# Performance work log

Measured on AMD Instinct MI355X. Metric: run time of the kernel, lower is better.

The kernel has to match this reference:

```python
import jax, jax.numpy as jnp
import numpy as np

N_ITERS = 50

def sinkhorn_knopp(W, n_iters=N_ITERS):
    # Project W onto the Birkhoff polytope via alternating row/col normalization.
    W = jnp.abs(W) + 1e-8
    def body(i, W):
        W = W / jnp.sum(W, axis=-1, keepdims=True)  # row-normalize
        W = W / jnp.sum(W, axis=-2, keepdims=True)  # col-normalize
        return W
    return jax.lax.fori_loop(0, n_iters, body, W)

def setup_inputs() -> dict:
    key = jax.random.key(0)
    k1, k2, k3 = jax.random.split(key, 3)
    residual = jax.random.normal(k1, (2, 4096, 4096), dtype=jnp.float32)
    sublayer_out = jax.random.normal(k2, (2, 4096, 4096), dtype=jnp.float32)
    # Mimic init: eye(2)*2 + 0.01*randn
    W_raw = jnp.eye(2, dtype=jnp.float32) * 2.0 + 0.01 * jax.random.normal(k3, (2, 2), dtype=jnp.float32)
    return {"residual": residual, "sublayer_out": sublayer_out, "W_raw": W_raw}

def reference(residual, sublayer_out, W_raw):
    W = sinkhorn_knopp(W_raw, N_ITERS)
    # stream_0 + stream_1 = (W00+W10)*residual + (W01+W11)*sublayer_out
    a = W[0, 0] + W[1, 0]
    b = W[0, 1] + W[1, 1]
    return a * residual + b * sublayer_out
```

## Files before the change

kernel.cpp:

```cpp
#include <hip/hip_runtime.h>


typedef float f4 __attribute__((ext_vector_type(4)));

#define SK_ITERS 50
constexpr int BLOCK = 256;
constexpr int VPT   = 8;
constexpr int CPB   = BLOCK * VPT;

__device__ __forceinline__ void sinkhorn_ab(const float* __restrict__ W,
                                            float& a, float& b) {
    float w00 = fabsf(W[0]) + 1e-8f;
    float w01 = fabsf(W[1]) + 1e-8f;
    float w10 = fabsf(W[2]) + 1e-8f;
    float w11 = fabsf(W[3]) + 1e-8f;
    #pragma unroll 1
    for (int i = 0; i < SK_ITERS; ++i) {
        float t0 = 1.0f / (w00 + w01);
        float t1 = 1.0f / (w10 + w11);
        w00 *= t0; w01 *= t0; w10 *= t1; w11 *= t1;
        float u0 = 1.0f / (w00 + w10);
        float u1 = 1.0f / (w01 + w11);
        w00 *= u0; w10 *= u0; w01 *= u1; w11 *= u1;
    }
    a = w00 + w10;
    b = w01 + w11;
}

__global__ __launch_bounds__(BLOCK) void sinkhorn_mix_kernel(
    const f4* __restrict__ r4, const f4* __restrict__ s4, f4* __restrict__ o4,
    const float* __restrict__ W_raw,
    const float* __restrict__ rs, const float* __restrict__ ss,
    float* __restrict__ os,
    long long n4, long long n)
{
    __shared__ float s_ab[2];

    const long long blockStart = (long long)blockIdx.x * CPB;
    const long long tbase      = blockStart + threadIdx.x;
    const bool full = (blockStart + CPB) <= n4;

    f4 rv[VPT], sv[VPT];

    if (full) {
        #pragma unroll
        for (int k = 0; k < VPT; ++k) rv[k] = r4[tbase + (long long)k * BLOCK];
        #pragma unroll
        for (int k = 0; k < VPT; ++k) sv[k] = s4[tbase + (long long)k * BLOCK];
    }

    if (threadIdx.x == 0) {
        float a, b;
        sinkhorn_ab(W_raw, a, b);
        s_ab[0] = a; s_ab[1] = b;
    }
    __syncthreads();
    const float a = s_ab[0], b = s_ab[1];

    if (full) {
        #pragma unroll
        for (int k = 0; k < VPT; ++k) {
            f4 ov;
            ov.x = a * rv[k].x + b * sv[k].x;
            ov.y = a * rv[k].y + b * sv[k].y;
            ov.z = a * rv[k].z + b * sv[k].z;
            ov.w = a * rv[k].w + b * sv[k].w;
            __builtin_nontemporal_store(ov, &o4[tbase + (long long)k * BLOCK]);
        }
    } else {
        #pragma unroll 1
        for (int k = 0; k < VPT; ++k) {
            long long i = tbase + (long long)k * BLOCK;
            if (i < n4) {
                f4 rvk = r4[i], svk = s4[i];
                f4 ov;
                ov.x = a * rvk.x + b * svk.x;
                ov.y = a * rvk.y + b * svk.y;
                ov.z = a * rvk.z + b * svk.z;
                ov.w = a * rvk.w + b * svk.w;
                o4[i] = ov;
            }
        }
        if (blockIdx.x == (int)gridDim.x - 1) {
            for (long long e = 4 * n4 + threadIdx.x; e < n; e += BLOCK) {
                os[e] = a * rs[e] + b * ss[e];
            }
        }
    }
}

extern "C" void kernel_launch(void* const* d_in, const int* in_sizes, int n_in,
                              void* d_out, int out_size, void* d_ws, size_t ws_size,
                              hipStream_t stream) {
    const float* residual = (const float*)d_in[0];
    const float* sublayer = (const float*)d_in[1];
    const float* W_raw    = (const float*)d_in[2];
    float* out            = (float*)d_out;

    const long long n  = (long long)out_size;
    const long long n4 = n >> 2;

    long long grid = (n4 + CPB - 1) / CPB;
    if (grid < 1) grid = 1;

    sinkhorn_mix_kernel<<<(int)grid, BLOCK, 0, stream>>>(
        (const f4*)residual, (const f4*)sublayer, (f4*)out, W_raw,
        residual, sublayer, out, n4, n);
}
```

Measured before the change: 323.8 us.

## Use grid-stride persistent blocks with per-thread Sinkhorn and 32-bit indexing

Replaces the one-shot grid of 8-vector-per-thread blocks with a capped grid of 2048 blocks that loop grid-stride over 4 vectors per thread per iteration. Every thread now computes the 2x2 Sinkhorn coefficients redundantly, which removes the shared-memory handoff and the block barrier. Indexing is switched to 32-bit ints to cut address arithmetic. This trades fewer loads in flight per iteration and loop overhead for less per-block setup and no sync; the 32-bit index limits the supported problem size.

```diff
diff --git a/kernel.cpp b/kernel.cpp
--- a/kernel.cpp
+++ b/kernel.cpp
@@ -5,15 +5,23 @@
 
 #define SK_ITERS 50
 constexpr int BLOCK = 256;
-constexpr int VPT   = 8;
-constexpr int CPB   = BLOCK * VPT;
+constexpr int BATCH = 4;
+constexpr int SPAN  = BLOCK * BATCH;
 
-__device__ __forceinline__ void sinkhorn_ab(const float* __restrict__ W,
-                                            float& a, float& b) {
-    float w00 = fabsf(W[0]) + 1e-8f;
-    float w01 = fabsf(W[1]) + 1e-8f;
-    float w10 = fabsf(W[2]) + 1e-8f;
-    float w11 = fabsf(W[3]) + 1e-8f;
+__global__ __launch_bounds__(BLOCK, 8) void sinkhorn_mix_kernel(
+    const f4* __restrict__ r4, const f4* __restrict__ s4, f4* __restrict__ o4,
+    const float* __restrict__ W_raw,
+    const float* __restrict__ rs, const float* __restrict__ ss,
+    float* __restrict__ os,
+    int n4, long long n)
+{
+    const int tid = threadIdx.x;
+
+    const f4 w = *reinterpret_cast<const f4*>(W_raw);
+    float w00 = fabsf(w.x) + 1e-8f;
+    float w01 = fabsf(w.y) + 1e-8f;
+    float w10 = fabsf(w.z) + 1e-8f;
+    float w11 = fabsf(w.w) + 1e-8f;
     #pragma unroll 1
     for (int i = 0; i < SK_ITERS; ++i) {
         float t0 = 1.0f / (w00 + w01);
@@ -23,68 +31,56 @@
         float u1 = 1.0f / (w01 + w11);
         w00 *= u0; w10 *= u0; w01 *= u1; w11 *= u1;
     }
-    a = w00 + w10;
-    b = w01 + w11;
-}
+    const float a = w00 + w10;
+    const float b = w01 + w11;
 
-__global__ __launch_bounds__(BLOCK) void sinkhorn_mix_kernel(
-    const f4* __restrict__ r4, const f4* __restrict__ s4, f4* __restrict__ o4,
-    const float* __restrict__ W_raw,
-    const float* __restrict__ rs, const float* __restrict__ ss,
-    float* __restrict__ os,
-    long long n4, long long n)
-{
-    __shared__ float s_ab[2];
+    const int stride = (int)gridDim.x * SPAN;
 
-    const long long blockStart = (long long)blockIdx.x * CPB;
-    const long long tbase      = blockStart + threadIdx.x;
-    const bool full = (blockStart + CPB) <= n4;
+    for (int base = (int)blockIdx.x * SPAN + tid; base < n4; base += stride) {
+        if (base + 3 * BLOCK < n4) {
+            f4 r0 = r4[base];
+            f4 r1 = r4[base +     BLOCK];
+            f4 r2 = r4[base + 2 * BLOCK];
+            f4 r3 = r4[base + 3 * BLOCK];
+            f4 s0 = s4[base];
+            f4 s1 = s4[base +     BLOCK];
+            f4 s2 = s4[base + 2 * BLOCK];
+            f4 s3 = s4[base + 3 * BLOCK];
 
-    f4 rv[VPT], sv[VPT];
+            f4 o0, o1, o2, o3;
+            o0.x = a * r0.x + b * s0.x; o0.y = a * r0.y + b * s0.y;
+            o0.z = a * r0.z + b * s0.z; o0.w = a * r0.w + b * s0.w;
+            o1.x = a * r1.x + b * s1.x; o1.y = a * r1.y + b * s1.y;
+            o1.z = a * r1.z + b * s1.z; o1.w = a * r1.w + b * s1.w;
+            o2.x = a * r2.x + b * s2.x; o2.y = a * r2.y + b * s2.y;
+            o2.z = a * r2.z + b * s2.z; o2.w = a * r2.w + b * s2.w;
+            o3.x = a * r3.x + b * s3.x; o3.y = a * r3.y + b * s3.y;
+            o3.z = a * r3.z + b * s3.z; o3.w = a * r3.w + b * s3.w;
 
-    if (full) {
-        #pragma unroll
-        for (int k = 0; k < VPT; ++k) rv[k] = r4[tbase + (long long)k * BLOCK];
-        #pragma unroll
-        for (int k = 0; k < VPT; ++k) sv[k] = s4[tbase + (long long)k * BLOCK];
+            __builtin_nontemporal_store(o0, &o4[base]);
+            __builtin_nontemporal_store(o1, &o4[base +     BLOCK]);
+            __builtin_nontemporal_store(o2, &o4[base + 2 * BLOCK]);
+            __builtin_nontemporal_store(o3, &o4[base + 3 * BLOCK]);
+        } else {
+            #pragma unroll
+            for (int k = 0; k < BATCH; ++k) {
+                int i = base + k * BLOCK;
+                if (i < n4) {
+                    f4 rv = r4[i], sv = s4[i];
+                    f4 ov;
+                    ov.x = a * rv.x + b * sv.x;
+                    ov.y = a * rv.y + b * sv.y;
+                    ov.z = a * rv.z + b * sv.z;
+                    ov.w = a * rv.w + b * sv.w;
+                    __builtin_nontemporal_store(ov, &o4[i]);
+                }
+            }
+        }
     }
 
-    if (threadIdx.x == 0) {
-        float a, b;
-        sinkhorn_ab(W_raw, a, b);
-        s_ab[0] = a; s_ab[1] = b;
-    }
-    __syncthreads();
-    const float a = s_ab[0], b = s_ab[1];
-
-    if (full) {
-        #pragma unroll
-        for (int k = 0; k < VPT; ++k) {
-            f4 ov;
-            ov.x = a * rv[k].x + b * sv[k].x;
-            ov.y = a * rv[k].y + b * sv[k].y;
-            ov.z = a * rv[k].z + b * sv[k].z;
-            ov.w = a * rv[k].w + b * sv[k].w;
-            __builtin_nontemporal_store(ov, &o4[tbase + (long long)k * BLOCK]);
-        }
-    } else {
-        #pragma unroll 1
-        for (int k = 0; k < VPT; ++k) {
-            long long i = tbase + (long long)k * BLOCK;
-            if (i < n4) {
-                f4 rvk = r4[i], svk = s4[i];
-                f4 ov;
-                ov.x = a * rvk.x + b * svk.x;
-                ov.y = a * rvk.y + b * svk.y;
-                ov.z = a * rvk.z + b * svk.z;
-                ov.w = a * rvk.w + b * svk.w;
-                o4[i] = ov;
-            }
-        }
-        if (blockIdx.x == (int)gridDim.x - 1) {
-            for (long long e = 4 * n4 + threadIdx.x; e < n; e += BLOCK) {
-                os[e] = a * rs[e] + b * ss[e];
-            }
+    if (blockIdx.x == 0) {
+        for (long long e = 4LL * n4 + tid; e < n; e += BLOCK) {
+            os[e] = a * rs[e] + b * ss[e];
         }
     }
 }
@@ -98,12 +94,12 @@
     float* out            = (float*)d_out;
 
     const long long n  = (long long)out_size;
-    const long long n4 = n >> 2;
+    const int       n4 = (int)(n >> 2);
 
-    long long grid = (n4 + CPB - 1) / CPB;
-    if (grid < 1) grid = 1;
+    long long needed = ((long long)n4 + SPAN - 1) / SPAN;
+    int grid = (int)((needed < 2048) ? (needed < 1 ? 1 : needed) : 2048);
 
-    sinkhorn_mix_kernel<<<(int)grid, BLOCK, 0, stream>>>(
+    sinkhorn_mix_kernel<<<grid, BLOCK, 0, stream>>>(
         (const f4*)residual, (const f4*)sublayer, (f4*)out, W_raw,
         residual, sublayer, out, n4, n);
 }
```

After: 325.1 us. About the same (+0.4%).
